# Kernel optimization log

Measured on AMD Instinct MI355X. Metric: run time of the kernel, lower is better.

## Reference

```python
import jax, jax.numpy as jnp
import numpy as np

EPS = 1e-6
NUM_HEADS = 8
HEAD_DIM = 64
ROPE_BASE = 100.0


def _rope_cos_sin(dim, height, width, base=ROPE_BASE):
    quarter = dim // 4
    inv_freq = 1.0 / (base ** (jnp.arange(quarter, dtype=jnp.float32) / quarter))
    freqs_y = jnp.arange(height, dtype=jnp.float32)[:, None] * inv_freq  # (H, q)
    emb_y = jnp.concatenate([freqs_y, freqs_y], axis=-1)                 # (H, dim//2)
    freqs_x = jnp.arange(width, dtype=jnp.float32)[:, None] * inv_freq
    emb_x = jnp.concatenate([freqs_x, freqs_x], axis=-1)                 # (W, dim//2)
    emb_y_grid = jnp.broadcast_to(emb_y[:, None, :], (height, width, dim // 2))
    emb_x_grid = jnp.broadcast_to(emb_x[None, :, :], (height, width, dim // 2))
    full = jnp.concatenate([emb_y_grid, emb_x_grid], axis=-1).reshape(-1, dim)  # (H*W, dim)
    return jnp.cos(full), jnp.sin(full)


def _rotate_half(x):
    x1, x2 = jnp.split(x, 2, axis=-1)
    return jnp.concatenate([-x2, x1], axis=-1)


def setup_inputs() -> dict:
    key = jax.random.key(0)
    ks = jax.random.split(key, 8)
    B, C, H, W = 16, 512, 32, 32
    t_dim = 512
    inner = NUM_HEADS * HEAD_DIM  # 512
    s = 0.02
    return {
        "x": jax.random.normal(ks[0], (B, C, H, W), dtype=jnp.float32),
        "time_emb": jax.random.normal(ks[1], (B, t_dim), dtype=jnp.float32),
        "tm_w1": jax.random.normal(ks[2], (t_dim, t_dim), dtype=jnp.float32) * s,
        "tm_b1": jnp.zeros((t_dim,), dtype=jnp.float32),
        "tm_w2": jax.random.normal(ks[3], (t_dim, 2 * C), dtype=jnp.float32) * s,
        "tm_b2": jnp.zeros((2 * C,), dtype=jnp.float32),
        "qkv_w": jax.random.normal(ks[4], (C, 3 * inner), dtype=jnp.float32) * s,
        "out_w": jax.random.normal(ks[5], (inner, C), dtype=jnp.float32) * s,
        "out_b": jnp.zeros((C,), dtype=jnp.float32),
    }


def reference(x, time_emb, tm_w1, tm_b1, tm_w2, tm_b2, qkv_w, out_w, out_b):
    B, C, H, W = x.shape
    N = H * W
    h, d = NUM_HEADS, HEAD_DIM

    # AdaCLN: channel-wise layernorm with time-conditioned affine modulation
    u = jnp.mean(x, axis=1, keepdims=True)
    s = jnp.mean((x - u) ** 2, axis=1, keepdims=True)
    x_norm = (x - u) / jnp.sqrt(s + EPS)
    emb = jax.nn.silu(time_emb @ tm_w1 + tm_b1) @ tm_w2 + tm_b2  # (B, 2C)
    gamma, beta = jnp.split(emb, 2, axis=1)
    x_norm = x_norm * (1.0 + gamma[:, :, None, None]) + beta[:, :, None, None]

    # (B, C, H, W) -> (B, N, C)
    tokens = x_norm.transpose(0, 2, 3, 1).reshape(B, N, C)

    qkv = tokens @ qkv_w  # (B, N, 3*inner)
    q, k, v = jnp.split(qkv, 3, axis=-1)
    q = q.reshape(B, N, h, d).transpose(0, 2, 1, 3)  # (B, h, N, d)
    k = k.reshape(B, N, h, d).transpose(0, 2, 1, 3)
    v = v.reshape(B, N, h, d).transpose(0, 2, 1, 3)

    cos, sin = _rope_cos_sin(d, H, W)  # (N, d)
    q = q * cos + _rotate_half(q) * sin
    k = k * cos + _rotate_half(k) * sin

    # SDPA, scale = 1/sqrt(head_dim)
    scale = 1.0 / jnp.sqrt(jnp.asarray(d, dtype=q.dtype))
    scores = jnp.einsum("bhqd,bhkd->bhqk", q, k) * scale
    attn = jax.nn.softmax(scores, axis=-1)
    out = jnp.einsum("bhqk,bhkd->bhqd", attn, v)  # (B, h, N, d)

    out = out.transpose(0, 2, 1, 3).reshape(B, N, h * d)
    out = out @ out_w + out_b  # (B, N, C)
    out = out.reshape(B, H, W, C).transpose(0, 3, 1, 2)
    return x + out
```

## Files before the change

kernel.cpp:

```cpp
#include <hip/hip_runtime.h>
#include <stdint.h>
#include <stddef.h>

#define B_  16
#define C_  512
#define N_  1024
#define NH  8
#define HD  64

typedef __attribute__((ext_vector_type(8))) short bf16x8;
typedef __attribute__((ext_vector_type(4))) float f32x4;
typedef __attribute__((ext_vector_type(2))) __bf16 bf16x2t;
typedef __attribute__((ext_vector_type(2))) unsigned uint2v;

__device__ __forceinline__ float bf2f(short s) {
    unsigned u = ((unsigned)(unsigned short)s) << 16;
    return __builtin_bit_cast(float, u);
}
__device__ __forceinline__ unsigned packcvt(float lo, float hi) {
    bf16x2t v = { (__bf16)lo, (__bf16)hi };
    return __builtin_bit_cast(unsigned, v);
}
__device__ __forceinline__ short f2bf_hw(float f) {
    __bf16 b = (__bf16)f;
    return __builtin_bit_cast(short, b);
}
__device__ __forceinline__ float fexp2(float x) {
#if __has_builtin(__builtin_amdgcn_exp2f)
    return __builtin_amdgcn_exp2f(x);
#else
    return exp2f(x);
#endif
}
__device__ __forceinline__ void plswap32(unsigned& a, unsigned& b) {
#if __has_builtin(__builtin_amdgcn_permlane32_swap)
    uint2v r = __builtin_amdgcn_permlane32_swap(a, b, false, false);
    a = r.x; b = r.y;
#else
    unsigned ax = (unsigned)__shfl_xor((int)a, 32, 64), bx = (unsigned)__shfl_xor((int)b, 32, 64);
    bool hi = (threadIdx.x & 32) != 0;
    unsigned na = hi ? bx : a, nb = hi ? b : ax;
    a = na; b = nb;
#endif
}
__device__ __forceinline__ void plswap16(unsigned& a, unsigned& b) {
#if __has_builtin(__builtin_amdgcn_permlane16_swap)
    uint2v r = __builtin_amdgcn_permlane16_swap(a, b, false, false);
    a = r.x; b = r.y;
#else
    unsigned ax = (unsigned)__shfl_xor((int)a, 16, 64), bx = (unsigned)__shfl_xor((int)b, 16, 64);
    bool hi = (threadIdx.x & 16) != 0;
    unsigned na = hi ? bx : a, nb = hi ? b : ax;
    a = na; b = nb;
#endif
}
__device__ __forceinline__ float bcf(unsigned u) { return __builtin_bit_cast(float, u); }
__device__ __forceinline__ unsigned bcu(float f) { return __builtin_bit_cast(unsigned, f); }
__device__ __forceinline__ float redsum_lg(float x) {
    unsigned a = bcu(x), b = a; plswap32(a, b);
    float s = bcf(a) + bcf(b);
    a = bcu(s); b = a; plswap16(a, b);
    return bcf(a) + bcf(b);
}

#define MFMA16(a, b, c) __builtin_amdgcn_mfma_f32_16x16x32_bf16((a), (b), (c), 0, 0, 0)

typedef __attribute__((address_space(3))) unsigned int lds_u32;
typedef __attribute__((address_space(1))) unsigned int glb_u32;
__device__ __forceinline__ void gload16(const void* g, void* l) {
    __builtin_amdgcn_global_load_lds((const glb_u32*)g, (lds_u32*)l, 16, 0, 0);
}

__global__ __launch_bounds__(256) void k_prep(
        const float* __restrict__ qkv_w, const float* __restrict__ out_w,
        short* __restrict__ qkvwT, short* __restrict__ outwT,
        float4* __restrict__ ropetab) {
    int bid = blockIdx.x, tid = threadIdx.x;
    if (bid < 256) {
        const float* src; short* dst; int J, jt, kt;
        if (bid < 192) { src = qkv_w; dst = qkvwT; J = 1536; jt = (bid % 24) * 64; kt = (bid / 24) * 64; }
        else { int b2 = bid - 192; src = out_w; dst = outwT; J = 512; jt = (b2 & 7) * 64; kt = (b2 >> 3) * 64; }
        __shared__ float ts[64][65];
        int r = tid >> 4, c4 = (tid & 15) * 4;
        for (int rr = 0; rr < 64; rr += 16) {
            float4 v = *(const float4*)(src + (size_t)(kt + rr + r) * J + jt + c4);
            ts[c4 + 0][rr + r] = v.x;
            ts[c4 + 1][rr + r] = v.y;
            ts[c4 + 2][rr + r] = v.z;
            ts[c4 + 3][rr + r] = v.w;
        }
        __syncthreads();
        int jr = tid >> 2, kc = (tid & 3) * 16;
        unsigned w[8];
#pragma unroll
        for (int i = 0; i < 8; i++) w[i] = packcvt(ts[jr][kc + 2 * i], ts[jr][kc + 2 * i + 1]);
        short* dp = dst + (size_t)(jt + jr) * 512 + kt + kc;
        *(uint4*)(dp)     = make_uint4(w[0], w[1], w[2], w[3]);
        *(uint4*)(dp + 8) = make_uint4(w[4], w[5], w[6], w[7]);
    } else {
        int idx = (bid - 256) * 256 + tid;
        int n = idx >> 5, dq = idx & 31, i = dq & 15;
        float w = powf(100.0f, -(float)i * (1.0f / 16.0f));
        float y = (float)(n >> 5), xx = (float)(n & 31);
        ropetab[idx] = make_float4(cosf(y * w), sinf(y * w), cosf(xx * w), sinf(xx * w));
    }
}

__global__ __launch_bounds__(256) void k_mlp1(
        const float* __restrict__ temb, const float* __restrict__ w1, const float* __restrict__ b1,
        float* __restrict__ h) {
    int b = blockIdx.y, jt = blockIdx.x, tid = threadIdx.x;
    int jl = tid & 31, j = jt * 32 + jl, ks = tid >> 5;
    __shared__ float tl[512];
    __shared__ float ps[8][32];
    tl[tid] = temb[b * 512 + tid];
    tl[tid + 256] = temb[b * 512 + tid + 256];
    __syncthreads();
    float acc = 0.f;
    const float* wp = w1 + (size_t)(ks * 64) * 512 + j;
#pragma unroll 8
    for (int kk = 0; kk < 64; kk++) acc += tl[ks * 64 + kk] * wp[(size_t)kk * 512];
    ps[ks][jl] = acc;
    __syncthreads();
    if (tid < 32) {
        float s = ((ps[0][tid] + ps[1][tid]) + (ps[2][tid] + ps[3][tid]))
                + ((ps[4][tid] + ps[5][tid]) + (ps[6][tid] + ps[7][tid]));
        s += b1[jt * 32 + tid];
        h[b * 512 + jt * 32 + tid] = s / (1.0f + __expf(-s));
    }
}

__global__ __launch_bounds__(256) void k_mlp2(
        const float* __restrict__ h, const float* __restrict__ w2, const float* __restrict__ b2,
        float* __restrict__ gbout) {
    int b = blockIdx.y, jt = blockIdx.x, tid = threadIdx.x;
    int jl = tid & 31, j = jt * 32 + jl, ks = tid >> 5;
    __shared__ float hl[512];
    __shared__ float ps[8][32];
    hl[tid] = h[b * 512 + tid];
    hl[tid + 256] = h[b * 512 + tid + 256];
    __syncthreads();
    float acc = 0.f;
    const float* wp = w2 + (size_t)(ks * 64) * 1024 + j;
#pragma unroll 8
    for (int kk = 0; kk < 64; kk++) acc += hl[ks * 64 + kk] * wp[(size_t)kk * 1024];
    ps[ks][jl] = acc;
    __syncthreads();
    if (tid < 32) {
        float s = ((ps[0][tid] + ps[1][tid]) + (ps[2][tid] + ps[3][tid]))
                + ((ps[4][tid] + ps[5][tid]) + (ps[6][tid] + ps[7][tid]));
        gbout[b * 1024 + jt * 32 + tid] = s + b2[jt * 32 + tid];
    }
}

__global__ __launch_bounds__(256) void k_adacln(
        const float* __restrict__ x, const float* __restrict__ gb, short* __restrict__ tokens) {
    int b = blockIdx.y, n0 = blockIdx.x * 64;
    int tid = threadIdx.x, pix = tid & 63, sl = tid >> 6;
    const float* xb = x + (size_t)b * C_ * N_;
    __shared__ float rs[4][64], rq[4][64], mean_s[64], rstd_s[64];
    __shared__ float xs[64][65];

    float sum = 0.f, sq = 0.f;
    for (int ci = 0; ci < 128; ci++) {
        int c = sl * 128 + ci;
        float v = xb[(size_t)c * N_ + n0 + pix];
        sum += v; sq += v * v;
    }
    rs[sl][pix] = sum; rq[sl][pix] = sq;
    __syncthreads();
    if (tid < 64) {
        float s1 = rs[0][tid] + rs[1][tid] + rs[2][tid] + rs[3][tid];
        float s2 = rq[0][tid] + rq[1][tid] + rq[2][tid] + rq[3][tid];
        float mu = s1 * (1.0f / 512.0f);
        float var = s2 * (1.0f / 512.0f) - mu * mu;
        mean_s[tid] = mu;
        rstd_s[tid] = rsqrtf(var + 1e-6f);
    }
    const float* gam = gb + b * 1024;
    const float* bet = gam + 512;
    int ch = tid & 7;
    for (int ct = 0; ct < 8; ct++) {
        __syncthreads();
        for (int it = 0; it < 16; it++) {
            int cl = it * 4 + sl;
            xs[cl][pix] = xb[(size_t)(ct * 64 + cl) * N_ + n0 + pix];
        }
        __syncthreads();
#pragma unroll
        for (int pp = 0; pp < 2; pp++) {
            int p = pp * 32 + (tid >> 3);
            float mu = mean_s[p], rt = rstd_s[p];
            float v[8];
#pragma unroll
            for (int j = 0; j < 8; j++) {
                int c = ct * 64 + ch * 8 + j;
                v[j] = (xs[ch * 8 + j][p] - mu) * rt * (1.0f + gam[c]) + bet[c];
            }
            uint4 ov = make_uint4(packcvt(v[0], v[1]), packcvt(v[2], v[3]),
                                  packcvt(v[4], v[5]), packcvt(v[6], v[7]));
            *(uint4*)(tokens + ((size_t)(b * N_ + n0 + p)) * C_ + ct * 64 + ch * 8) = ov;
        }
    }
}

__global__ __launch_bounds__(256) void k_gemm_qkv(
        const short* __restrict__ A, const short* __restrict__ Bt,
        const float4* __restrict__ ropetab,
        short* __restrict__ qr, short* __restrict__ kr, short* __restrict__ vt) {
    __shared__ short Asm[128 * 32];
    __shared__ short Bsm[128 * 32];
    int tid = threadIdx.x, wv = tid >> 6, ln = tid & 63;
    int wr = wv >> 1, wc = wv & 1, lr = ln & 15, lg = ln >> 4;
    const short* Ab = A + (size_t)blockIdx.y * 128 * 512;
    const short* Bb = Bt + (size_t)blockIdx.x * 128 * 512;
    f32x4 acc[4][4] = {};
    int srow = ln >> 2, sch = ln & 3;
    for (int kb = 0; kb < 512; kb += 32) {
        int r0 = wv * 32;
        const short* ga = Ab + (size_t)(r0 + srow) * 512 + kb + sch * 8;
        gload16(ga, (void*)(Asm + r0 * 32));
        gload16(ga + 16 * 512, (void*)(Asm + (r0 + 16) * 32));
        const short* gbp = Bb + (size_t)(r0 + srow) * 512 + kb + sch * 8;
        gload16(gbp, (void*)(Bsm + r0 * 32));
        gload16(gbp + 16 * 512, (void*)(Bsm + (r0 + 16) * 32));
        __syncthreads();
        bf16x8 af[4], bfr[4];
#pragma unroll
        for (int m = 0; m < 4; m++) af[m] = *(const bf16x8*)(Asm + (wr * 64 + m * 16 + lr) * 32 + lg * 8);
#pragma unroll
        for (int f = 0; f < 4; f++) bfr[f] = *(const bf16x8*)(Bsm + (wc * 64 + f * 16 + lr) * 32 + lg * 8);
#pragma unroll
        for (int m = 0; m < 4; m++)
#pragma unroll
            for (int f = 0; f < 4; f++)
                acc[m][f] = MFMA16(af[m], bfr[f], acc[m][f]);
        __syncthreads();
    }
    int mbase = blockIdx.y * 128;
    int sec = blockIdx.x >> 2;
    int h = (2 * blockIdx.x + wc) & 7;
    if (sec < 2) {
        short* dst0 = (sec == 0) ? qr : kr;
#pragma unroll
        for (int m = 0; m < 4; m++) {
            int gmb = mbase + wr * 64 + m * 16 + lg * 4;
#pragma unroll
            for (int r = 0; r < 4; r++) {
                int gm = gmb + r; int b = gm >> 10, n = gm & 1023;
                short* rowp = dst0 + (((size_t)b * NH + h) * N_ + n) * HD;
                const float4* tr = ropetab + n * 32;
#pragma unroll
                for (int f2 = 0; f2 < 2; f2++) {
                    int d_lo = f2 * 16 + lr;
                    float4 t = tr[d_lo];
                    float a = acc[m][f2][r], bb2 = acc[m][f2 + 2][r];
                    rowp[d_lo]      = f2bf_hw(a * t.x - bb2 * t.y);
                    rowp[d_lo + 32] = f2bf_hw(bb2 * t.z + a * t.w);
                }
            }
        }
    } else {
#pragma unroll
        for (int m = 0; m < 4; m++) {
            int gmb = mbase + wr * 64 + m * 16 + lg * 4;
            int b = gmb >> 10, n0 = gmb & 1023;
#pragma unroll
            for (int f = 0; f < 4; f++) {
                int d = f * 16 + lr;
                uint2 val;
                val.x = packcvt(acc[m][f][0], acc[m][f][1]);
                val.y = packcvt(acc[m][f][2], acc[m][f][3]);
                *(uint2*)(vt + (((size_t)b * NH + h) * HD + d) * N_ + n0) = val;
            }
        }
    }
}

__global__ __launch_bounds__(256) void k_flash8(
        const short* __restrict__ qr, const short* __restrict__ kr, const short* __restrict__ vt,
        short* __restrict__ attn_out) {
    __shared__ short Ks[2][4096];
    __shared__ short Vs[2][4096];
    int bh = blockIdx.x, b = bh >> 3, h = bh & 7;
    int qt = blockIdx.y;
    int tid = threadIdx.x, wv = tid >> 6, ln = tid & 63;
    int lr = ln & 15, lg = ln >> 4;
    const short* Qb = qr + ((size_t)bh * N_ + qt * 128 + wv * 32) * HD;
    const short* Kb = kr + (size_t)bh * N_ * HD;
    const short* Vb = vt + (size_t)bh * HD * N_;

    const float QSCALE = 0.125f * 1.44269504f;
    bf16x8 qf[2][2];
#pragma unroll
    for (int qg = 0; qg < 2; qg++)
#pragma unroll
        for (int hf = 0; hf < 2; hf++) {
            bf16x8 raw = *(const bf16x8*)(Qb + (qg * 16 + lr) * 64 + hf * 32 + lg * 8);
            bf16x8 sc;
#pragma unroll
            for (int j = 0; j < 8; j++) sc[j] = f2bf_hw(bf2f(raw[j]) * QSCALE);
            qf[qg][hf] = sc;
        }

    int srow = ln >> 3, cpos = ln & 7;

    float l_part[2] = {0.f, 0.f};
    f32x4 ao[2][4] = {};

#pragma unroll
    for (int p = 0; p < 2; p++) {
        int rloc = p * 32 + wv * 8 + srow;
        int csrc = cpos ^ (rloc & 7);
        gload16(Kb + ((size_t)rloc) * 64 + csrc * 8, (void*)&Ks[0][(p * 32 + wv * 8) * 64]);
        gload16(Vb + ((size_t)rloc) * 1024 + csrc * 8, (void*)&Vs[0][(p * 32 + wv * 8) * 64]);
    }
    __syncthreads();

    for (int kt = 0; kt < 16; kt++) {
        int cur = kt & 1;
        if (kt < 15) {
            int nxt = cur ^ 1, ktn = kt + 1;
#pragma unroll
            for (int p = 0; p < 2; p++) {
                int rloc = p * 32 + wv * 8 + srow;
                int csrc = cpos ^ (rloc & 7);
                gload16(Kb + ((size_t)(ktn * 64 + rloc)) * 64 + csrc * 8,
                        (void*)&Ks[nxt][(p * 32 + wv * 8) * 64]);
                gload16(Vb + ((size_t)rloc) * 1024 + ktn * 64 + csrc * 8,
                        (void*)&Vs[nxt][(p * 32 + wv * 8) * 64]);
            }
        }

        f32x4 sT[2][4];
#pragma unroll
        for (int f = 0; f < 4; f++) {
            int r = f * 16 + lr;
            const short* kp = &Ks[cur][r * 64];
            bf16x8 ka  = *(const bf16x8*)(kp + ((lg ^ (r & 7)) * 8));
            bf16x8 kb2 = *(const bf16x8*)(kp + (((4 + lg) ^ (r & 7)) * 8));
#pragma unroll
            for (int qg = 0; qg < 2; qg++) {
                f32x4 s = {};
                s = MFMA16(ka, qf[qg][0], s);
                s = MFMA16(kb2, qf[qg][1], s);
                sT[qg][f] = s;
            }
        }

        union U4 { unsigned u[4]; bf16x8 v; };
        U4 pb[2][2];
#pragma unroll
        for (int qg = 0; qg < 2; qg++) {
            float rsum = 0.f;
            unsigned pk[4][2];
#pragma unroll
            for (int f = 0; f < 4; f++) {
                float p0 = fexp2(sT[qg][f][0]);
                float p1 = fexp2(sT[qg][f][1]);
                float p2 = fexp2(sT[qg][f][2]);
                float p3 = fexp2(sT[qg][f][3]);
                rsum += (p0 + p1) + (p2 + p3);
                pk[f][0] = packcvt(p0, p1);
                pk[f][1] = packcvt(p2, p3);
            }
            l_part[qg] += rsum;

#pragma unroll
            for (int kb = 0; kb < 2; kb++) {
                unsigned a = pk[2 * kb][0], c = pk[2 * kb + 1][0];
                plswap32(a, c); plswap16(a, c);
                pb[qg][kb].u[0] = a; pb[qg][kb].u[2] = c;
                unsigned bb = pk[2 * kb][1], d = pk[2 * kb + 1][1];
                plswap32(bb, d); plswap16(bb, d);
                pb[qg][kb].u[1] = bb; pb[qg][kb].u[3] = d;
            }
        }

#pragma unroll
        for (int dt = 0; dt < 4; dt++) {
            int rr = dt * 16 + lr;
            const short* vp = &Vs[cur][rr * 64];
            bf16x8 va0 = *(const bf16x8*)(vp + ((lg ^ (rr & 7)) * 8));
            bf16x8 va1 = *(const bf16x8*)(vp + (((4 + lg) ^ (rr & 7)) * 8));
#pragma unroll
            for (int qg = 0; qg < 2; qg++) {
                ao[qg][dt] = MFMA16(va0, pb[qg][0].v, ao[qg][dt]);
                ao[qg][dt] = MFMA16(va1, pb[qg][1].v, ao[qg][dt]);
            }
        }
        __syncthreads();
    }

#pragma unroll
    for (int qg = 0; qg < 2; qg++) {
        float inv = 1.0f / redsum_lg(l_part[qg]);
        int qglob = qt * 128 + wv * 32 + qg * 16 + lr;
        size_t ob = ((size_t)b * N_ + qglob) * 512 + h * 64 + lg * 4;
#pragma unroll
        for (int dt = 0; dt < 4; dt++) {
            uint2 val;
            val.x = packcvt(ao[qg][dt][0] * inv, ao[qg][dt][1] * inv);
            val.y = packcvt(ao[qg][dt][2] * inv, ao[qg][dt][3] * inv);
            *(uint2*)(attn_out + ob + dt * 16) = val;
        }
    }
}

__global__ __launch_bounds__(256) void k_gemm_out(
        const short* __restrict__ A, const short* __restrict__ Bt,
        const float* __restrict__ x, const float* __restrict__ obias, float* __restrict__ out) {
    __shared__ short Asm[128 * 32];
    __shared__ short Bsm[128 * 32];
    int tid = threadIdx.x, wv = tid >> 6, ln = tid & 63;
    int wr = wv >> 1, wc = wv & 1, lr = ln & 15, lg = ln >> 4;
    const short* Ab = A + (size_t)blockIdx.y * 128 * 512;
    const short* Bb = Bt + (size_t)blockIdx.x * 128 * 512;
    f32x4 acc[4][4] = {};
    int srow = ln >> 2, sch = ln & 3;
    for (int kb = 0; kb < 512; kb += 32) {
        int r0 = wv * 32;
        const short* ga = Ab + (size_t)(r0 + srow) * 512 + kb + sch * 8;
        gload16(ga, (void*)(Asm + r0 * 32));
        gload16(ga + 16 * 512, (void*)(Asm + (r0 + 16) * 32));
        const short* gbp = Bb + (size_t)(r0 + srow) * 512 + kb + sch * 8;
        gload16(gbp, (void*)(Bsm + r0 * 32));
        gload16(gbp + 16 * 512, (void*)(Bsm + (r0 + 16) * 32));
        __syncthreads();
        bf16x8 af[4], bfr[4];
#pragma unroll
        for (int m = 0; m < 4; m++) af[m] = *(const bf16x8*)(Asm + (wr * 64 + m * 16 + lr) * 32 + lg * 8);
#pragma unroll
        for (int f = 0; f < 4; f++) bfr[f] = *(const bf16x8*)(Bsm + (wc * 64 + f * 16 + lr) * 32 + lg * 8);
#pragma unroll
        for (int m = 0; m < 4; m++)
#pragma unroll
            for (int f = 0; f < 4; f++)
                acc[m][f] = MFMA16(af[m], bfr[f], acc[m][f]);
        __syncthreads();
    }
    int cb = blockIdx.y * 128 + wr * 64, tb = blockIdx.x * 128 + wc * 64;
#pragma unroll
    for (int m = 0; m < 4; m++) {
#pragma unroll
        for (int f = 0; f < 4; f++) {
            int gt = tb + f * 16 + lr;
            int b = gt >> 10, n = gt & 1023;
#pragma unroll
            for (int r = 0; r < 4; r++) {
                int gc = cb + m * 16 + lg * 4 + r;
                size_t ad = ((size_t)b * C_ + gc) * N_ + n;
                out[ad] = acc[m][f][r] + obias[gc] + x[ad];
            }
        }
    }
}

extern "C" void kernel_launch(void* const* d_in, const int* in_sizes, int n_in,
                              void* d_out, int out_size, void* d_ws, size_t ws_size,
                              hipStream_t stream) {
    const float* x     = (const float*)d_in[0];
    const float* temb  = (const float*)d_in[1];
    const float* tm_w1 = (const float*)d_in[2];
    const float* tm_b1 = (const float*)d_in[3];
    const float* tm_w2 = (const float*)d_in[4];
    const float* tm_b2 = (const float*)d_in[5];
    const float* qkv_w = (const float*)d_in[6];
    const float* out_w = (const float*)d_in[7];
    const float* out_b = (const float*)d_in[8];
    float* out = (float*)d_out;

    char* ws = (char*)d_ws;
    short*  qkvwT  = (short*)(ws);
    short*  outwT  = (short*)(ws + 1572864);
    float4* ropetab= (float4*)(ws + 2097152);
    float*  gb     = (float*)(ws + 2621440);
    short*  tokens = (short*)(ws + 2686976);
    short*  qr     = (short*)(ws + 19464192);
    short*  kr     = (short*)(ws + 36241408);
    short*  vt     = (short*)(ws + 53018624);
    short*  attn   = tokens;
    float*  hbuf   = (float*)(ws + 2686976);

    k_prep<<<dim3(384), dim3(256), 0, stream>>>(qkv_w, out_w, qkvwT, outwT, ropetab);
    k_mlp1<<<dim3(16, 16), dim3(256), 0, stream>>>(temb, tm_w1, tm_b1, hbuf);
    k_mlp2<<<dim3(32, 16), dim3(256), 0, stream>>>(hbuf, tm_w2, tm_b2, gb);
    k_adacln<<<dim3(16, 16), dim3(256), 0, stream>>>(x, gb, tokens);
    k_gemm_qkv<<<dim3(12, 128), dim3(256), 0, stream>>>(tokens, qkvwT, ropetab, qr, kr, vt);
    k_flash8<<<dim3(128, 8), dim3(256), 0, stream>>>(qr, kr, vt, attn);
    k_gemm_out<<<dim3(128, 4), dim3(256), 0, stream>>>(outwT, attn, x, out_b, out);
}
```

Measured before the change: 156.3 us.

## Triple-buffer K/V tiles in flash attention with prefetch distance two

Shared-memory K/V staging in the attention kernel goes from double to triple buffering, so loads are issued two tiles ahead. The full __syncthreads is replaced with explicit vmcnt waits that keep the newest tile's loads in flight, plus a raw s_barrier. The aim is to hide more global-load latency behind the MFMA work. In exchange it uses 50% more LDS per block, which may reduce occupancy, and its correctness relies on hand-counted outstanding vmem operations.

New measurement: 151.1 us. 3.3% less time.

```diff
diff --git a/kernel.cpp b/kernel.cpp
--- a/kernel.cpp
+++ b/kernel.cpp
@@ -277,11 +277,11 @@
     }
 }
 
-__global__ __launch_bounds__(256) void k_flash8(
+__global__ __launch_bounds__(256) void k_flash9(
         const short* __restrict__ qr, const short* __restrict__ kr, const short* __restrict__ vt,
         short* __restrict__ attn_out) {
-    __shared__ short Ks[2][4096];
-    __shared__ short Vs[2][4096];
+    __shared__ short Ks[3][4096];
+    __shared__ short Vs[3][4096];
     int bh = blockIdx.x, b = bh >> 3, h = bh & 7;
     int qt = blockIdx.y;
     int tid = threadIdx.x, wv = tid >> 6, ln = tid & 63;
@@ -308,19 +308,29 @@
     float l_part[2] = {0.f, 0.f};
     f32x4 ao[2][4] = {};
 
-#pragma unroll
-    for (int p = 0; p < 2; p++) {
-        int rloc = p * 32 + wv * 8 + srow;
-        int csrc = cpos ^ (rloc & 7);
-        gload16(Kb + ((size_t)rloc) * 64 + csrc * 8, (void*)&Ks[0][(p * 32 + wv * 8) * 64]);
-        gload16(Vb + ((size_t)rloc) * 1024 + csrc * 8, (void*)&Vs[0][(p * 32 + wv * 8) * 64]);
-    }
-    __syncthreads();
+    asm volatile("s_waitcnt vmcnt(0)" ::: "memory");
+    __builtin_amdgcn_sched_barrier(0);
+
+#pragma unroll
+    for (int t0 = 0; t0 < 2; t0++) {
+#pragma unroll
+        for (int p = 0; p < 2; p++) {
+            int rloc = p * 32 + wv * 8 + srow;
+            int csrc = cpos ^ (rloc & 7);
+            gload16(Kb + ((size_t)(t0 * 64 + rloc)) * 64 + csrc * 8,
+                    (void*)&Ks[t0][(p * 32 + wv * 8) * 64]);
+            gload16(Vb + ((size_t)rloc) * 1024 + t0 * 64 + csrc * 8,
+                    (void*)&Vs[t0][(p * 32 + wv * 8) * 64]);
+        }
+    }
+    asm volatile("s_waitcnt vmcnt(4)" ::: "memory");
+    __builtin_amdgcn_s_barrier();
+    __builtin_amdgcn_sched_barrier(0);
 
     for (int kt = 0; kt < 16; kt++) {
-        int cur = kt & 1;
-        if (kt < 15) {
-            int nxt = cur ^ 1, ktn = kt + 1;
+        int cur = kt % 3;
+        if (kt < 14) {
+            int nxt = (kt + 2) % 3, ktn = kt + 2;
 #pragma unroll
             for (int p = 0; p < 2; p++) {
                 int rloc = p * 32 + wv * 8 + srow;
@@ -389,7 +399,13 @@
                 ao[qg][dt] = MFMA16(va1, pb[qg][1].v, ao[qg][dt]);
             }
         }
-        __syncthreads();
+
+        if (kt < 15) {
+            if (kt < 14) asm volatile("s_waitcnt vmcnt(4)" ::: "memory");
+            else         asm volatile("s_waitcnt vmcnt(0)" ::: "memory");
+            __builtin_amdgcn_s_barrier();
+            __builtin_amdgcn_sched_barrier(0);
+        }
     }
 
 #pragma unroll
@@ -487,6 +503,6 @@
     k_mlp2<<<dim3(32, 16), dim3(256), 0, stream>>>(hbuf, tm_w2, tm_b2, gb);
     k_adacln<<<dim3(16, 16), dim3(256), 0, stream>>>(x, gb, tokens);
     k_gemm_qkv<<<dim3(12, 128), dim3(256), 0, stream>>>(tokens, qkvwT, ropetab, qr, kr, vt);
-    k_flash8<<<dim3(128, 8), dim3(256), 0, stream>>>(qr, kr, vt, attn);
+    k_flash9<<<dim3(128, 8), dim3(256), 0, stream>>>(qr, kr, vt, attn);
     k_gemm_out<<<dim3(128, 4), dim3(256), 0, stream>>>(outwT, attn, x, out_b, out);
 }
```
